# Optimization experiments

Hardware: AMD Instinct MI355X
Metric: run time of the kernel (lower is better)

## Reference

```python
import jax, jax.numpy as jnp
import numpy as np

NUM_HEADING_BIN = 12
NUM_SIZE_CLUSTER = 8
DELTA_NORM_W = 0.01
CENTER_W = 0.5
B, N = 4096, 2048


def huber(err, delta=1.0):
    a = jnp.abs(err)
    q = jnp.minimum(a, delta)
    return jnp.mean(0.5 * q * q + delta * (a - q))


def box3d_corners(centers, headings, sizes):
    # centers (B,3), headings (B,), sizes (B,3) -> (B,8,3)
    l, w, h = sizes[:, 0:1], sizes[:, 1:2], sizes[:, 2:3]
    sx = jnp.asarray([1, 1, -1, -1, 1, 1, -1, -1], dtype=sizes.dtype)
    sy = jnp.asarray([1, -1, -1, 1, 1, -1, -1, 1], dtype=sizes.dtype)
    sz = jnp.asarray([1, 1, 1, 1, -1, -1, -1, -1], dtype=sizes.dtype)
    corners = jnp.stack([0.5 * l * sx, 0.5 * w * sy, 0.5 * h * sz], axis=1)  # (B,3,8)
    c, s = jnp.cos(headings), jnp.sin(headings)
    z, o = jnp.zeros_like(c), jnp.ones_like(c)
    R = jnp.stack([jnp.stack([c, -s, z], -1),
                   jnp.stack([s, c, z], -1),
                   jnp.stack([z, z, o], -1)], axis=1)  # (B,3,3)
    out = jnp.einsum('bij,bjk->bik', R, corners) + centers[:, :, None]
    return jnp.transpose(out, (0, 2, 1))  # (B,8,3)


def setup_inputs() -> dict:
    key = jax.random.key(0)
    ks = jax.random.split(key, 9)
    return {
        'mask_xyz_mean': jax.random.normal(ks[0], (B, 3), jnp.float32),
        'point_cloud': jax.random.normal(ks[1], (B, 3, N), jnp.float32),
        'x_delta': jax.random.normal(ks[2], (B, 3, N), jnp.float32),
        'center_label': jax.random.normal(ks[3], (B, 3), jnp.float32),
        'size_residual_label': jax.random.normal(ks[4], (B, 3), jnp.float32),
        'heading_residual_label': jax.random.normal(ks[5], (B,), jnp.float32),
        'mean_sizes': jax.random.uniform(ks[6], (NUM_SIZE_CLUSTER, 3), jnp.float32, 0.5, 2.5),
        'size_class_label': jax.random.randint(ks[7], (B,), 0, NUM_SIZE_CLUSTER, jnp.int32),
        'heading_class_label': jax.random.randint(ks[8], (B,), 0, NUM_HEADING_BIN, jnp.int32),
    }


def reference(mask_xyz_mean, point_cloud, x_delta, center_label,
              size_residual_label, heading_residual_label, mean_sizes,
              size_class_label, heading_class_label):
    eps = 0.0  # faithful: original has no eps
    # center loss
    center_dist = jnp.linalg.norm(mask_xyz_mean - center_label, axis=1)
    center_loss = CENTER_W * huber(center_dist)

    # label assembly (onehot-sum == gather)
    size_label = mean_sizes[size_class_label] + size_residual_label  # (B,3)
    bin_centers = jnp.arange(0, np.pi, np.pi / NUM_HEADING_BIN, dtype=jnp.float32)
    heading_label = heading_residual_label + bin_centers[heading_class_label]  # (B,)

    corners_3d_gt = box3d_corners(center_label, heading_label, size_label)
    corners_2d_gt = corners_3d_gt[:, 4:8, :2]  # (B,4,2)

    v = center_label[:, :2]  # (B,2)
    p_dir = jnp.stack([-v[:, 1], v[:, 0]], axis=1)
    p_dir = p_dir / jnp.linalg.norm(p_dir, axis=1, keepdims=True)  # (B,2)

    pp_label = jnp.einsum('bkc,bc->bk', corners_2d_gt, p_dir)  # (B,4)
    py_max, py_min = jnp.max(pp_label, axis=1), jnp.min(pp_label, axis=1)
    std_y_label = (py_max - py_min) / 4
    mean_y_label = (py_max + py_min) / 2

    v_norm = jnp.linalg.norm(v, axis=1, keepdims=True)  # (B,1)
    proj_label = jnp.einsum('bkc,bc->bk', corners_2d_gt, v) / v_norm  # (B,4)
    p_max, p_min = jnp.max(proj_label, axis=1), jnp.min(proj_label, axis=1)
    std_label = (p_max - p_min) / 4
    mean_label = (p_max + p_min) / 2

    pc_xy = jnp.transpose(point_cloud, (0, 2, 1))[:, :, :2]  # (B,N,2)

    pp_pc = jnp.einsum('bnc,bc->bn', pc_xy, p_dir)  # (B,N)
    std_y_pc = jnp.std(pp_pc, axis=1, ddof=1)
    mean_y_pc = jnp.mean(pp_pc, axis=1)
    y_std_loss = huber(jnp.abs(std_y_label - std_y_pc))
    y_mean_loss = huber(jnp.abs(mean_y_label - mean_y_pc))

    proj_pc = jnp.einsum('bnc,bc->bn', pc_xy, v) / v_norm  # (B,N)
    std_pc = jnp.std(proj_pc, axis=1, ddof=1)
    mean_pc = jnp.mean(proj_pc, axis=1)
    x_std_loss = huber(jnp.abs(std_label - std_pc))
    x_mean_loss = huber(jnp.abs(mean_label - mean_pc))

    delta_norm = jnp.sqrt(jnp.sum(x_delta * x_delta, axis=(1, 2)))
    delta_norm_loss = DELTA_NORM_W * huber(delta_norm)

    total = center_loss + x_std_loss + x_mean_loss + delta_norm_loss + y_mean_loss + y_std_loss
    return 0.4 * total
```

## Files before the change

kernel.cpp:

```cpp
#include <hip/hip_runtime.h>
#include <math.h>

#define B_SZ 4096
#define N_PTS 2048
#define BLOCK 256
#define WPB (BLOCK / 64)

__device__ __forceinline__ float huber1(float a) {
    float q = fminf(a, 1.0f);
    return 0.5f * q * q + (a - q);
}

__global__ __launch_bounds__(BLOCK, 4) void loss_stage1(
    const float* __restrict__ mask_xyz_mean,
    const float* __restrict__ point_cloud,
    const float* __restrict__ x_delta,
    const float* __restrict__ center_label,
    const float* __restrict__ size_residual,
    const float* __restrict__ heading_residual,
    const float* __restrict__ mean_sizes,
    const int*   __restrict__ size_class,
    const int*   __restrict__ heading_class,
    float* __restrict__ ws)
{
    const int wave = threadIdx.x >> 6;
    const int lane = threadIdx.x & 63;
    const int b    = blockIdx.x * WPB + wave;

    const float cx = center_label[b * 3 + 0];
    const float cy = center_label[b * 3 + 1];

    const float vnorm2 = cx * cx + cy * cy;
    const float vnorm  = sqrtf(vnorm2);
    const float pdx = -cy / vnorm;
    const float pdy =  cx / vnorm;

    const size_t base = (size_t)b * 3 * N_PTS;
    const float4* px4 = (const float4*)(point_cloud + base);
    const float4* py4 = (const float4*)(point_cloud + base + N_PTS);
    const float4* pd4 = (const float4*)(x_delta + base);

    float s_pp = 0.f, s_pp2 = 0.f, s_t = 0.f, s_t2 = 0.f, s_d2 = 0.f;

    #pragma unroll
    for (int k = 0; k < N_PTS / 4 / 64; ++k) {
        const int i = lane + k * 64;
        const float4 x4 = px4[i];
        const float4 y4 = py4[i];
        {
            float pp = x4.x * pdx + y4.x * pdy;
            float t  = x4.x * cx  + y4.x * cy;
            s_pp += pp; s_pp2 += pp * pp; s_t += t; s_t2 += t * t;
        }
        {
            float pp = x4.y * pdx + y4.y * pdy;
            float t  = x4.y * cx  + y4.y * cy;
            s_pp += pp; s_pp2 += pp * pp; s_t += t; s_t2 += t * t;
        }
        {
            float pp = x4.z * pdx + y4.z * pdy;
            float t  = x4.z * cx  + y4.z * cy;
            s_pp += pp; s_pp2 += pp * pp; s_t += t; s_t2 += t * t;
        }
        {
            float pp = x4.w * pdx + y4.w * pdy;
            float t  = x4.w * cx  + y4.w * cy;
            s_pp += pp; s_pp2 += pp * pp; s_t += t; s_t2 += t * t;
        }
    }

    #pragma unroll
    for (int k = 0; k < 3 * N_PTS / 4 / 64; ++k) {
        const float4 d = pd4[lane + k * 64];
        s_d2 += d.x * d.x + d.y * d.y + d.z * d.z + d.w * d.w;
    }

    #pragma unroll
    for (int off = 32; off > 0; off >>= 1) {
        s_pp  += __shfl_down(s_pp,  off, 64);
        s_pp2 += __shfl_down(s_pp2, off, 64);
        s_t   += __shfl_down(s_t,   off, 64);
        s_t2  += __shfl_down(s_t2,  off, 64);
        s_d2  += __shfl_down(s_d2,  off, 64);
    }

    if (lane == 0) {
        const float mx = mask_xyz_mean[b * 3 + 0];
        const float my = mask_xyz_mean[b * 3 + 1];
        const float mz = mask_xyz_mean[b * 3 + 2];
        const float cz = center_label[b * 3 + 2];
        const float dxc = mx - cx, dyc = my - cy, dzc = mz - cz;
        const float center_dist = sqrtf(dxc * dxc + dyc * dyc + dzc * dzc);

        const int sc = size_class[b];
        const float l  = mean_sizes[sc * 3 + 0] + size_residual[b * 3 + 0];
        const float w_ = mean_sizes[sc * 3 + 1] + size_residual[b * 3 + 1];

        const float theta = heading_residual[b] +
                            (float)heading_class[b] * (float)(M_PI / 12.0);
        const float c = cosf(theta);
        const float s = sinf(theta);
        const float hl = 0.5f * l, hw = 0.5f * w_;

        float X[4], Y[4];
        X[0] =  c * hl - s * hw + cx;  Y[0] =  s * hl + c * hw + cy;
        X[1] =  c * hl + s * hw + cx;  Y[1] =  s * hl - c * hw + cy;
        X[2] = -c * hl + s * hw + cx;  Y[2] = -s * hl - c * hw + cy;
        X[3] = -c * hl - s * hw + cx;  Y[3] = -s * hl + c * hw + cy;

        float ppmax = -INFINITY, ppmin = INFINITY;
        float pmax  = -INFINITY, pmin  = INFINITY;
        #pragma unroll
        for (int k = 0; k < 4; ++k) {
            const float pp = X[k] * pdx + Y[k] * pdy;
            const float pj = (X[k] * cx + Y[k] * cy) / vnorm;
            ppmax = fmaxf(ppmax, pp); ppmin = fminf(ppmin, pp);
            pmax  = fmaxf(pmax,  pj); pmin  = fminf(pmin,  pj);
        }
        const float std_y_label  = (ppmax - ppmin) * 0.25f;
        const float mean_y_label = (ppmax + ppmin) * 0.5f;
        const float std_label    = (pmax - pmin) * 0.25f;
        const float mean_label   = (pmax + pmin) * 0.5f;

        const float invN   = 1.0f / (float)N_PTS;
        const float invNm1 = 1.0f / (float)(N_PTS - 1);

        const float mean_y_pc = s_pp * invN;
        const float var_y = (s_pp2 - s_pp * s_pp * invN) * invNm1;
        const float std_y_pc = sqrtf(fmaxf(var_y, 0.0f));

        const float mean_pc = (s_t * invN) / vnorm;
        const float var_x = ((s_t2 - s_t * s_t * invN) * invNm1) / vnorm2;
        const float std_pc = sqrtf(fmaxf(var_x, 0.0f));

        const float delta_norm = sqrtf(s_d2);

        const float total =
              0.5f  * huber1(center_dist)
            +         huber1(fabsf(std_label  - std_pc))
            +         huber1(fabsf(mean_label - mean_pc))
            + 0.01f * huber1(delta_norm)
            +         huber1(fabsf(mean_y_label - mean_y_pc))
            +         huber1(fabsf(std_y_label  - std_y_pc));

        ws[b] = total;
    }
}

__global__ __launch_bounds__(BLOCK) void loss_stage2(
    const float* __restrict__ ws, float* __restrict__ out)
{
    const int tid = threadIdx.x;
    const float4* w4 = (const float4*)ws;

    float s = 0.f;
    #pragma unroll
    for (int k = 0; k < B_SZ / 4 / BLOCK; ++k) {
        const float4 v = w4[tid + k * BLOCK];
        s += v.x + v.y + v.z + v.w;
    }

    #pragma unroll
    for (int off = 32; off > 0; off >>= 1)
        s += __shfl_down(s, off, 64);

    __shared__ float red[BLOCK / 64];
    const int wave = tid >> 6;
    const int lane = tid & 63;
    if (lane == 0) red[wave] = s;
    __syncthreads();

    if (tid == 0) {
        #pragma unroll
        for (int w = 1; w < BLOCK / 64; ++w) s += red[w];
        out[0] = s * (0.4f / (float)B_SZ);
    }
}

extern "C" void kernel_launch(void* const* d_in, const int* in_sizes, int n_in,
                              void* d_out, int out_size, void* d_ws, size_t ws_size,
                              hipStream_t stream) {
    const float* mask_xyz_mean    = (const float*)d_in[0];
    const float* point_cloud      = (const float*)d_in[1];
    const float* x_delta          = (const float*)d_in[2];
    const float* center_label     = (const float*)d_in[3];
    const float* size_residual    = (const float*)d_in[4];
    const float* heading_residual = (const float*)d_in[5];
    const float* mean_sizes       = (const float*)d_in[6];
    const int*   size_class       = (const int*)d_in[7];
    const int*   heading_class    = (const int*)d_in[8];
    float* ws  = (float*)d_ws;
    float* out = (float*)d_out;

    loss_stage1<<<B_SZ / WPB, BLOCK, 0, stream>>>(
        mask_xyz_mean, point_cloud, x_delta, center_label, size_residual,
        heading_residual, mean_sizes, size_class, heading_class, ws);
    loss_stage2<<<1, BLOCK, 0, stream>>>(ws, out);
}
```

Baseline: 225.3 us.

## Split per-batch sweep into flat chunked partial reductions plus finalize kernel

```diff
diff --git a/kernel.cpp b/kernel.cpp
--- a/kernel.cpp
+++ b/kernel.cpp
@@ -4,17 +4,88 @@
 #define B_SZ 4096
 #define N_PTS 2048
 #define BLOCK 256
-#define WPB (BLOCK / 64)
+#define SWEEP_BLOCKS 2048
+#define XD_ITERS 12
+#define PC_ITERS 4
+
+#define WS_PC  0
+#define WS_XD  131072
+#define WS_TOT (131072 + 98304)
 
 __device__ __forceinline__ float huber1(float a) {
     float q = fminf(a, 1.0f);
     return 0.5f * q * q + (a - q);
 }
 
-__global__ __launch_bounds__(BLOCK, 4) void loss_stage1(
-    const float* __restrict__ mask_xyz_mean,
+__global__ __launch_bounds__(BLOCK, 8) void sweep(
     const float* __restrict__ point_cloud,
     const float* __restrict__ x_delta,
+    const float* __restrict__ center_label,
+    float* __restrict__ ws)
+{
+    const int tid  = threadIdx.x;
+    const int wave = tid >> 6;
+    const int lane = tid & 63;
+
+    if (blockIdx.x < SWEEP_BLOCKS) {
+        const int s = blockIdx.x;
+        const float4* xd4 = (const float4*)x_delta;
+        float* __restrict__ wxd = ws + WS_XD;
+        #pragma unroll
+        for (int k = 0; k < XD_ITERS; ++k) {
+            const int W = s + k * SWEEP_BLOCKS;
+            const float4 d = xd4[(size_t)W * 256 + tid];
+            float v = d.x * d.x + d.y * d.y + d.z * d.z + d.w * d.w;
+            #pragma unroll
+            for (int off = 32; off > 0; off >>= 1)
+                v += __shfl_down(v, off, 64);
+            if (lane == 0) wxd[W * 4 + wave] = v;
+        }
+    } else {
+        const int s = blockIdx.x - SWEEP_BLOCKS;
+        const float4* pc4 = (const float4*)point_cloud;
+        float4* __restrict__ wpc = (float4*)(ws + WS_PC);
+        #pragma unroll
+        for (int k = 0; k < PC_ITERS; ++k) {
+            const int W = s + k * SWEEP_BLOCKS;
+            const int e = W >> 1;
+            const int h = W & 1;
+            const float cx = center_label[e * 3 + 0];
+            const float cy = center_label[e * 3 + 1];
+            const float vn  = sqrtf(cx * cx + cy * cy);
+            const float pdx = -cy / vn;
+            const float pdy =  cx / vn;
+
+            const size_t fx = (size_t)e * 1536 + h * 256 + tid;
+            const float4 x4 = pc4[fx];
+            const float4 y4 = pc4[fx + 512];
+
+            float s_pp = 0.f, s_pp2 = 0.f, s_t = 0.f, s_t2 = 0.f;
+            {
+                const float xs[4] = {x4.x, x4.y, x4.z, x4.w};
+                const float ys[4] = {y4.x, y4.y, y4.z, y4.w};
+                #pragma unroll
+                for (int j = 0; j < 4; ++j) {
+                    const float pp = xs[j] * pdx + ys[j] * pdy;
+                    const float t  = xs[j] * cx  + ys[j] * cy;
+                    s_pp += pp; s_pp2 += pp * pp; s_t += t; s_t2 += t * t;
+                }
+            }
+            #pragma unroll
+            for (int off = 32; off > 0; off >>= 1) {
+                s_pp  += __shfl_down(s_pp,  off, 64);
+                s_pp2 += __shfl_down(s_pp2, off, 64);
+                s_t   += __shfl_down(s_t,   off, 64);
+                s_t2  += __shfl_down(s_t2,  off, 64);
+            }
+            if (lane == 0)
+                wpc[W * 4 + wave] = make_float4(s_pp, s_pp2, s_t, s_t2);
+        }
+    }
+}
+
+__global__ __launch_bounds__(BLOCK) void finalize(
+    const float* __restrict__ mask_xyz_mean,
     const float* __restrict__ center_label,
     const float* __restrict__ size_residual,
     const float* __restrict__ heading_residual,
@@ -23,135 +94,96 @@
     const int*   __restrict__ heading_class,
     float* __restrict__ ws)
 {
-    const int wave = threadIdx.x >> 6;
-    const int lane = threadIdx.x & 63;
-    const int b    = blockIdx.x * WPB + wave;
-
-    const float cx = center_label[b * 3 + 0];
-    const float cy = center_label[b * 3 + 1];
-
+    const int e = blockIdx.x * BLOCK + threadIdx.x;
+
+    float s_pp = 0.f, s_pp2 = 0.f, s_t = 0.f, s_t2 = 0.f;
+    const float4* pcp = ((const float4*)(ws + WS_PC)) + (size_t)e * 8;
+    #pragma unroll
+    for (int i = 0; i < 8; ++i) {
+        const float4 p = pcp[i];
+        s_pp += p.x; s_pp2 += p.y; s_t += p.z; s_t2 += p.w;
+    }
+    float s_d2 = 0.f;
+    const float4* xdp = ((const float4*)(ws + WS_XD)) + (size_t)e * 6;
+    #pragma unroll
+    for (int i = 0; i < 6; ++i) {
+        const float4 p = xdp[i];
+        s_d2 += (p.x + p.y) + (p.z + p.w);
+    }
+
+    const float cx = center_label[e * 3 + 0];
+    const float cy = center_label[e * 3 + 1];
+    const float cz = center_label[e * 3 + 2];
     const float vnorm2 = cx * cx + cy * cy;
     const float vnorm  = sqrtf(vnorm2);
     const float pdx = -cy / vnorm;
     const float pdy =  cx / vnorm;
 
-    const size_t base = (size_t)b * 3 * N_PTS;
-    const float4* px4 = (const float4*)(point_cloud + base);
-    const float4* py4 = (const float4*)(point_cloud + base + N_PTS);
-    const float4* pd4 = (const float4*)(x_delta + base);
-
-    float s_pp = 0.f, s_pp2 = 0.f, s_t = 0.f, s_t2 = 0.f, s_d2 = 0.f;
-
-    #pragma unroll
-    for (int k = 0; k < N_PTS / 4 / 64; ++k) {
-        const int i = lane + k * 64;
-        const float4 x4 = px4[i];
-        const float4 y4 = py4[i];
-        {
-            float pp = x4.x * pdx + y4.x * pdy;
-            float t  = x4.x * cx  + y4.x * cy;
-            s_pp += pp; s_pp2 += pp * pp; s_t += t; s_t2 += t * t;
-        }
-        {
-            float pp = x4.y * pdx + y4.y * pdy;
-            float t  = x4.y * cx  + y4.y * cy;
-            s_pp += pp; s_pp2 += pp * pp; s_t += t; s_t2 += t * t;
-        }
-        {
-            float pp = x4.z * pdx + y4.z * pdy;
-            float t  = x4.z * cx  + y4.z * cy;
-            s_pp += pp; s_pp2 += pp * pp; s_t += t; s_t2 += t * t;
-        }
-        {
-            float pp = x4.w * pdx + y4.w * pdy;
-            float t  = x4.w * cx  + y4.w * cy;
-            s_pp += pp; s_pp2 += pp * pp; s_t += t; s_t2 += t * t;
-        }
-    }
-
-    #pragma unroll
-    for (int k = 0; k < 3 * N_PTS / 4 / 64; ++k) {
-        const float4 d = pd4[lane + k * 64];
-        s_d2 += d.x * d.x + d.y * d.y + d.z * d.z + d.w * d.w;
-    }
-
-    #pragma unroll
-    for (int off = 32; off > 0; off >>= 1) {
-        s_pp  += __shfl_down(s_pp,  off, 64);
-        s_pp2 += __shfl_down(s_pp2, off, 64);
-        s_t   += __shfl_down(s_t,   off, 64);
-        s_t2  += __shfl_down(s_t2,  off, 64);
-        s_d2  += __shfl_down(s_d2,  off, 64);
-    }
-
-    if (lane == 0) {
-        const float mx = mask_xyz_mean[b * 3 + 0];
-        const float my = mask_xyz_mean[b * 3 + 1];
-        const float mz = mask_xyz_mean[b * 3 + 2];
-        const float cz = center_label[b * 3 + 2];
-        const float dxc = mx - cx, dyc = my - cy, dzc = mz - cz;
-        const float center_dist = sqrtf(dxc * dxc + dyc * dyc + dzc * dzc);
-
-        const int sc = size_class[b];
-        const float l  = mean_sizes[sc * 3 + 0] + size_residual[b * 3 + 0];
-        const float w_ = mean_sizes[sc * 3 + 1] + size_residual[b * 3 + 1];
-
-        const float theta = heading_residual[b] +
-                            (float)heading_class[b] * (float)(M_PI / 12.0);
-        const float c = cosf(theta);
-        const float s = sinf(theta);
-        const float hl = 0.5f * l, hw = 0.5f * w_;
-
-        float X[4], Y[4];
-        X[0] =  c * hl - s * hw + cx;  Y[0] =  s * hl + c * hw + cy;
-        X[1] =  c * hl + s * hw + cx;  Y[1] =  s * hl - c * hw + cy;
-        X[2] = -c * hl + s * hw + cx;  Y[2] = -s * hl - c * hw + cy;
-        X[3] = -c * hl - s * hw + cx;  Y[3] = -s * hl + c * hw + cy;
-
-        float ppmax = -INFINITY, ppmin = INFINITY;
-        float pmax  = -INFINITY, pmin  = INFINITY;
-        #pragma unroll
-        for (int k = 0; k < 4; ++k) {
-            const float pp = X[k] * pdx + Y[k] * pdy;
-            const float pj = (X[k] * cx + Y[k] * cy) / vnorm;
-            ppmax = fmaxf(ppmax, pp); ppmin = fminf(ppmin, pp);
-            pmax  = fmaxf(pmax,  pj); pmin  = fminf(pmin,  pj);
-        }
-        const float std_y_label  = (ppmax - ppmin) * 0.25f;
-        const float mean_y_label = (ppmax + ppmin) * 0.5f;
-        const float std_label    = (pmax - pmin) * 0.25f;
-        const float mean_label   = (pmax + pmin) * 0.5f;
-
-        const float invN   = 1.0f / (float)N_PTS;
-        const float invNm1 = 1.0f / (float)(N_PTS - 1);
-
-        const float mean_y_pc = s_pp * invN;
-        const float var_y = (s_pp2 - s_pp * s_pp * invN) * invNm1;
-        const float std_y_pc = sqrtf(fmaxf(var_y, 0.0f));
-
-        const float mean_pc = (s_t * invN) / vnorm;
-        const float var_x = ((s_t2 - s_t * s_t * invN) * invNm1) / vnorm2;
-        const float std_pc = sqrtf(fmaxf(var_x, 0.0f));
-
-        const float delta_norm = sqrtf(s_d2);
-
-        const float total =
-              0.5f  * huber1(center_dist)
-            +         huber1(fabsf(std_label  - std_pc))
-            +         huber1(fabsf(mean_label - mean_pc))
-            + 0.01f * huber1(delta_norm)
-            +         huber1(fabsf(mean_y_label - mean_y_pc))
-            +         huber1(fabsf(std_y_label  - std_y_pc));
-
-        ws[b] = total;
-    }
-}
-
-__global__ __launch_bounds__(BLOCK) void loss_stage2(
+    const float mx = mask_xyz_mean[e * 3 + 0];
+    const float my = mask_xyz_mean[e * 3 + 1];
+    const float mz = mask_xyz_mean[e * 3 + 2];
+    const float dxc = mx - cx, dyc = my - cy, dzc = mz - cz;
+    const float center_dist = sqrtf(dxc * dxc + dyc * dyc + dzc * dzc);
+
+    const int sc = size_class[e];
+    const float l  = mean_sizes[sc * 3 + 0] + size_residual[e * 3 + 0];
+    const float w_ = mean_sizes[sc * 3 + 1] + size_residual[e * 3 + 1];
+
+    const float theta = heading_residual[e] +
+                        (float)heading_class[e] * (float)(M_PI / 12.0);
+    const float c = cosf(theta);
+    const float s = sinf(theta);
+    const float hl = 0.5f * l, hw = 0.5f * w_;
+
+    float X[4], Y[4];
+    X[0] =  c * hl - s * hw + cx;  Y[0] =  s * hl + c * hw + cy;
+    X[1] =  c * hl + s * hw + cx;  Y[1] =  s * hl - c * hw + cy;
+    X[2] = -c * hl + s * hw + cx;  Y[2] = -s * hl - c * hw + cy;
+    X[3] = -c * hl - s * hw + cx;  Y[3] = -s * hl + c * hw + cy;
+
+    float ppmax = -INFINITY, ppmin = INFINITY;
+    float pmax  = -INFINITY, pmin  = INFINITY;
+    #pragma unroll
+    for (int k = 0; k < 4; ++k) {
+        const float pp = X[k] * pdx + Y[k] * pdy;
+        const float pj = (X[k] * cx + Y[k] * cy) / vnorm;
+        ppmax = fmaxf(ppmax, pp); ppmin = fminf(ppmin, pp);
+        pmax  = fmaxf(pmax,  pj); pmin  = fminf(pmin,  pj);
+    }
+    const float std_y_label  = (ppmax - ppmin) * 0.25f;
+    const float mean_y_label = (ppmax + ppmin) * 0.5f;
+    const float std_label    = (pmax - pmin) * 0.25f;
+    const float mean_label   = (pmax + pmin) * 0.5f;
+
+    const float invN   = 1.0f / (float)N_PTS;
+    const float invNm1 = 1.0f / (float)(N_PTS - 1);
+
+    const float mean_y_pc = s_pp * invN;
+    const float var_y = (s_pp2 - s_pp * s_pp * invN) * invNm1;
+    const float std_y_pc = sqrtf(fmaxf(var_y, 0.0f));
+
+    const float mean_pc = (s_t * invN) / vnorm;
+    const float var_x = ((s_t2 - s_t * s_t * invN) * invNm1) / vnorm2;
+    const float std_pc = sqrtf(fmaxf(var_x, 0.0f));
+
+    const float delta_norm = sqrtf(s_d2);
+
+    const float total =
+          0.5f  * huber1(center_dist)
+        +         huber1(fabsf(std_label  - std_pc))
+        +         huber1(fabsf(mean_label - mean_pc))
+        + 0.01f * huber1(delta_norm)
+        +         huber1(fabsf(mean_y_label - mean_y_pc))
+        +         huber1(fabsf(std_y_label  - std_y_pc));
+
+    ws[WS_TOT + e] = total;
+}
+
+__global__ __launch_bounds__(BLOCK) void loss_reduce(
     const float* __restrict__ ws, float* __restrict__ out)
 {
     const int tid = threadIdx.x;
-    const float4* w4 = (const float4*)ws;
+    const float4* w4 = (const float4*)(ws + WS_TOT);
 
     float s = 0.f;
     #pragma unroll
@@ -192,8 +224,10 @@
     float* ws  = (float*)d_ws;
     float* out = (float*)d_out;
 
-    loss_stage1<<<B_SZ / WPB, BLOCK, 0, stream>>>(
-        mask_xyz_mean, point_cloud, x_delta, center_label, size_residual,
-        heading_residual, mean_sizes, size_class, heading_class, ws);
-    loss_stage2<<<1, BLOCK, 0, stream>>>(ws, out);
-}
+    sweep<<<2 * SWEEP_BLOCKS, BLOCK, 0, stream>>>(
+        point_cloud, x_delta, center_label, ws);
+    finalize<<<B_SZ / BLOCK, BLOCK, 0, stream>>>(
+        mask_xyz_mean, center_label, size_residual, heading_residual,
+        mean_sizes, size_class, heading_class, ws);
+    loss_reduce<<<1, BLOCK, 0, stream>>>(ws, out);
+}
```

After: 223.8 us. About the same (-0.7%).
